# Performance work log

Measured on AMD Instinct MI355X. Metric: run time of the kernel, lower is better.

The kernel has to match this reference:

```python
import jax, jax.numpy as jnp
import numpy as np
from jax import lax

WIN = 9  # window size per spatial dim


def setup_inputs() -> dict:
    key = jax.random.key(0)
    k1, k2 = jax.random.split(key)
    shape = (2, 1, 160, 192, 160)  # [B, C=1, D, H, W]
    y_true = jax.random.uniform(k1, shape, dtype=jnp.float32)
    y_pred = jax.random.uniform(k2, shape, dtype=jnp.float32)
    return {"y_true": y_true, "y_pred": y_pred}


def reference(y_true, y_pred):
    Ii, Ji = y_true, y_pred
    ndims = Ii.ndim - 2  # 3 for volumes
    pad = WIN // 2
    # all five maps in the channel dim: [B, 5, D, H, W]
    all_five = jnp.concatenate([Ii, Ji, Ii * Ii, Ji * Ji, Ii * Ji], axis=1)
    # grouped box-filter conv: ones kernel [O=5, I/g=1, 9,9,9]
    kernel = jnp.ones((5, 1) + (WIN,) * ndims, dtype=Ii.dtype)
    conv = lax.conv_general_dilated(
        all_five, kernel,
        window_strides=(1,) * ndims,
        padding=[(pad, pad)] * ndims,
        feature_group_count=5,
        dimension_numbers=("NCDHW", "OIDHW", "NCDHW"),
    )
    I_sum, J_sum, I2_sum, J2_sum, IJ_sum = jnp.split(conv, 5, axis=1)
    win_size = jnp.asarray(float(WIN), dtype=Ii.dtype)
    cross = IJ_sum - J_sum / win_size * I_sum
    I_var = I2_sum - I_sum / win_size * I_sum
    J_var = J2_sum - J_sum / win_size * J_sum
    cc = cross * cross / (I_var * J_var + 1e-5)
    return -jnp.mean(cc)
```

## Files before the change

### kernel.cpp

```cpp
#include <hip/hip_runtime.h>

#define B_ 2
#define D_ 160
#define H_ 192
#define W_ 160
#define W4_ (W_ / 4)
#define HW_ (H_ * W_)
#define DHW_ (D_ * HW_)
#define NV_ ((long long)B_ * D_ * H_ * W_)

#define XT 32
#define NXT (W_ / XT)
#define YCH1 6
#define NYC1 (H_ / YCH1)
#define SPAD 4

#define ROWS2 8
#define ZCH2 10
#define NZC2 (D_ / ZCH2)
#define PAD 4
#define LROW (W_ + 2 * PAD)

#define A_YSTRIDE ((size_t)5 * W_)
#define A_ZSTRIDE ((size_t)5 * HW_)

typedef _Float16 half4 __attribute__((ext_vector_type(4)));

__global__ void k_zero(double* acc) { *acc = 0.0; }

__device__ __forceinline__ void add4h(float4& d, const half4 v) {
    d.x += (float)v.x; d.y += (float)v.y; d.z += (float)v.z; d.w += (float)v.w;
}
__device__ __forceinline__ void sub4h(float4& d, const half4 v) {
    d.x -= (float)v.x; d.y -= (float)v.y; d.z -= (float)v.z; d.w -= (float)v.w;
}

template<int SGN>
__device__ __forceinline__ void acc_lds(float4 s[5], const half4 ha, const half4 hb) {
    const float4 a = make_float4((float)ha.x, (float)ha.y, (float)ha.z, (float)ha.w);
    const float4 b = make_float4((float)hb.x, (float)hb.y, (float)hb.z, (float)hb.w);
    if (SGN > 0) {
        s[0].x += a.x;     s[0].y += a.y;     s[0].z += a.z;     s[0].w += a.w;
        s[1].x += b.x;     s[1].y += b.y;     s[1].z += b.z;     s[1].w += b.w;
        s[2].x += a.x*a.x; s[2].y += a.y*a.y; s[2].z += a.z*a.z; s[2].w += a.w*a.w;
        s[3].x += b.x*b.x; s[3].y += b.y*b.y; s[3].z += b.z*b.z; s[3].w += b.w*b.w;
        s[4].x += a.x*b.x; s[4].y += a.y*b.y; s[4].z += a.z*b.z; s[4].w += a.w*b.w;
    } else {
        s[0].x -= a.x;     s[0].y -= a.y;     s[0].z -= a.z;     s[0].w -= a.w;
        s[1].x -= b.x;     s[1].y -= b.y;     s[1].z -= b.z;     s[1].w -= b.w;
        s[2].x -= a.x*a.x; s[2].y -= a.y*a.y; s[2].z -= a.z*a.z; s[2].w -= a.w*a.w;
        s[3].x -= b.x*b.x; s[3].y -= b.y*b.y; s[3].z -= b.z*b.z; s[3].w -= b.w*b.w;
        s[4].x -= a.x*b.x; s[4].y -= a.y*b.y; s[4].z -= a.z*b.z; s[4].w -= a.w*b.w;
    }
}

__global__ __launch_bounds__(256) void k1_ysum(const float* __restrict__ I,
                                               const float* __restrict__ J,
                                               _Float16* __restrict__ A) {
    __shared__ _Float16 sI[H_][XT + SPAD];
    __shared__ _Float16 sJ[H_][XT + SPAD];
    const int tid = threadIdx.x;
    const int xt  = blockIdx.x % NXT;
    const int bz  = blockIdx.x / NXT;
    const int x0  = xt * XT;

    const float* Ibase = I + (size_t)bz * HW_ + x0;
    const float* Jbase = J + (size_t)bz * HW_ + x0;

#pragma unroll
    for (int i = 0; i < 6; ++i) {
        const int idx = i * 256 + tid;
        const int row = idx >> 3;
        const int g   = idx & 7;
        const float4 vi = *(const float4*)(Ibase + (size_t)row * W_ + g * 4);
        const float4 vj = *(const float4*)(Jbase + (size_t)row * W_ + g * 4);
        half4 hi, hj;
        hi.x = (_Float16)vi.x; hi.y = (_Float16)vi.y; hi.z = (_Float16)vi.z; hi.w = (_Float16)vi.w;
        hj.x = (_Float16)vj.x; hj.y = (_Float16)vj.y; hj.z = (_Float16)vj.z; hj.w = (_Float16)vj.w;
        *(half4*)&sI[row][g * 4] = hi;
        *(half4*)&sJ[row][g * 4] = hj;
    }
    __syncthreads();

    const int xg = tid & 7;
    const int yc = tid >> 3;
    const int y0 = yc * YCH1;
    const int x4 = xg * 4;

    _Float16* Ap = A + (size_t)bz * A_ZSTRIDE + x0 + x4;

    float4 s[5];
#pragma unroll
    for (int c = 0; c < 5; ++c) s[c] = make_float4(0, 0, 0, 0);

#pragma unroll
    for (int j = 0; j < 8; ++j) {
        const int yin = y0 - 4 + j;
        if (yin >= 0)
            acc_lds<+1>(s, *(const half4*)&sI[yin][x4], *(const half4*)&sJ[yin][x4]);
    }
#pragma unroll
    for (int k = 0; k < YCH1; ++k) {
        const int yi = y0 + k + 4;
        if (yi < H_)
            acc_lds<+1>(s, *(const half4*)&sI[yi][x4], *(const half4*)&sJ[yi][x4]);
        const int yo = y0 + k - 5;
        if (yo >= 0)
            acc_lds<-1>(s, *(const half4*)&sI[yo][x4], *(const half4*)&sJ[yo][x4]);

        _Float16* Ay = Ap + (size_t)(y0 + k) * A_YSTRIDE;
#pragma unroll
        for (int c = 0; c < 5; ++c) {
            half4 h;
            h.x = (_Float16)s[c].x; h.y = (_Float16)s[c].y;
            h.z = (_Float16)s[c].z; h.w = (_Float16)s[c].w;
            *(half4*)(Ay + c * W_) = h;
        }
    }
}

__global__ void k2_zxcc(const _Float16* __restrict__ A, double* __restrict__ acc) {
    __shared__ float sbuf[ROWS2][5][LROW];
    __shared__ float red[512];
    const int tid = threadIdx.x;
    const int r   = tid / W4_;
    const int l   = tid - r * W4_;
    const int x4  = l * 4;
    const int blk = blockIdx.x;
    const int zc  = blk % NZC2;
    const int rp  = blk / NZC2;
    const int gy  = rp * ROWS2 + r;
    const int b   = gy / H_;
    const int yy  = gy - b * H_;
    const int z0  = zc * ZCH2;

    {
        float* p = &sbuf[0][0][0];
        for (int i = tid; i < ROWS2 * 5 * LROW; i += ROWS2 * W4_) p[i] = 0.f;
    }

    const _Float16* Abase = A + (size_t)b * D_ * A_ZSTRIDE + (size_t)yy * A_YSTRIDE + x4;

    float4 s[5];
#pragma unroll
    for (int c = 0; c < 5; ++c) s[c] = make_float4(0, 0, 0, 0);
#pragma unroll
    for (int j = 0; j < 8; ++j) {
        const int zi = z0 - 4 + j;
        if (zi >= 0) {
            const _Float16* Az = Abase + (size_t)zi * A_ZSTRIDE;
#pragma unroll
            for (int c = 0; c < 5; ++c)
                add4h(s[c], *(const half4*)(Az + c * W_));
        }
    }
    __syncthreads();

    float local = 0.f;
    for (int k = 0; k < ZCH2; ++k) {
        const int zi = z0 + k + 4;
        if (zi < D_) {
            const _Float16* Az = Abase + (size_t)zi * A_ZSTRIDE;
#pragma unroll
            for (int c = 0; c < 5; ++c)
                add4h(s[c], *(const half4*)(Az + c * W_));
        }
        const int zo = z0 + k - 5;
        if (zo >= 0) {
            const _Float16* Az = Abase + (size_t)zo * A_ZSTRIDE;
#pragma unroll
            for (int c = 0; c < 5; ++c)
                sub4h(s[c], *(const half4*)(Az + c * W_));
        }
#pragma unroll
        for (int c = 0; c < 5; ++c)
            *(float4*)&sbuf[r][c][PAD + x4] = s[c];
        __syncthreads();

        float4 S5[5];
#pragma unroll
        for (int c = 0; c < 5; ++c) {
            const float4 a0 = *(const float4*)&sbuf[r][c][x4];
            const float4 a1 = *(const float4*)&sbuf[r][c][x4 + 4];
            const float4 a2 = *(const float4*)&sbuf[r][c][x4 + 8];
            const float o0 = a0.x + a0.y + a0.z + a0.w + a1.x + a1.y + a1.z + a1.w + a2.x;
            const float o1 = o0 - a0.x + a2.y;
            const float o2 = o1 - a0.y + a2.z;
            const float o3 = o2 - a0.z + a2.w;
            S5[c] = make_float4(o0, o1, o2, o3);
        }
        const float inv9 = 1.0f / 9.0f;
        {
            const float cr = S5[4].x - S5[1].x * S5[0].x * inv9;
            const float iv = S5[2].x - S5[0].x * S5[0].x * inv9;
            const float jv = S5[3].x - S5[1].x * S5[1].x * inv9;
            local += cr * cr / (iv * jv + 1e-5f);
        }
        {
            const float cr = S5[4].y - S5[1].y * S5[0].y * inv9;
            const float iv = S5[2].y - S5[0].y * S5[0].y * inv9;
            const float jv = S5[3].y - S5[1].y * S5[1].y * inv9;
            local += cr * cr / (iv * jv + 1e-5f);
        }
        {
            const float cr = S5[4].z - S5[1].z * S5[0].z * inv9;
            const float iv = S5[2].z - S5[0].z * S5[0].z * inv9;
            const float jv = S5[3].z - S5[1].z * S5[1].z * inv9;
            local += cr * cr / (iv * jv + 1e-5f);
        }
        {
            const float cr = S5[4].w - S5[1].w * S5[0].w * inv9;
            const float iv = S5[2].w - S5[0].w * S5[0].w * inv9;
            const float jv = S5[3].w - S5[1].w * S5[1].w * inv9;
            local += cr * cr / (iv * jv + 1e-5f);
        }
        __syncthreads();
    }

    red[tid] = local;
    if (tid < 192) red[320 + tid] = 0.f;
    __syncthreads();
    for (int off = 256; off > 0; off >>= 1) {
        if (tid < off) red[tid] += red[tid + off];
        __syncthreads();
    }
    if (tid == 0) atomicAdd(acc, (double)red[0]);
}

__global__ void p_direct(const float* __restrict__ I, const float* __restrict__ J,
                         double* __restrict__ acc) {
    const long long idx = (long long)blockIdx.x * blockDim.x + threadIdx.x;
    float local = 0.f;
    if (idx < NV_) {
        const int x = (int)(idx % W_);
        long long t = idx / W_;
        const int y = (int)(t % H_);
        t /= H_;
        const int z = (int)(t % D_);
        const int b = (int)(t / D_);
        const int z0 = max(z - 4, 0), z1 = min(z + 4, D_ - 1);
        const int y0 = max(y - 4, 0), y1 = min(y + 4, H_ - 1);
        const int x0 = max(x - 4, 0), x1 = min(x + 4, W_ - 1);
        float sI = 0.f, sJ = 0.f, sI2 = 0.f, sJ2 = 0.f, sIJ = 0.f;
        for (int zz = z0; zz <= z1; ++zz)
            for (int yy = y0; yy <= y1; ++yy) {
                const size_t row = ((size_t)(b * D_ + zz) * H_ + yy) * W_;
                for (int xx = x0; xx <= x1; ++xx) {
                    const float a = I[row + xx];
                    const float bb = J[row + xx];
                    sI += a; sJ += bb; sI2 += a * a; sJ2 += bb * bb; sIJ += a * bb;
                }
            }
        const float inv9 = 1.0f / 9.0f;
        const float cross = sIJ - sJ * sI * inv9;
        const float iv    = sI2 - sI * sI * inv9;
        const float jv    = sJ2 - sJ * sJ * inv9;
        local = cross * cross / (iv * jv + 1e-5f);
    }
    __shared__ float red[256];
    red[threadIdx.x] = local;
    __syncthreads();
    for (int off = 128; off > 0; off >>= 1) {
        if (threadIdx.x < off) red[threadIdx.x] += red[threadIdx.x + off];
        __syncthreads();
    }
    if (threadIdx.x == 0) atomicAdd(acc, (double)red[0]);
}

__global__ void k_final(const double* __restrict__ acc, float* __restrict__ out) {
    out[0] = (float)(-(*acc) / (double)NV_);
}

extern "C" void kernel_launch(void* const* d_in, const int* in_sizes, int n_in,
                              void* d_out, int out_size, void* d_ws, size_t ws_size,
                              hipStream_t stream) {
    const float* I = (const float*)d_in[0];
    const float* J = (const float*)d_in[1];
    float* out = (float*)d_out;

    const size_t needA = (size_t)5 * B_ * DHW_ * sizeof(_Float16);
    if (ws_size >= 1024 + needA) {
        double* acc = (double*)d_ws;
        _Float16* A = (_Float16*)((char*)d_ws + 1024);
        k_zero<<<1, 1, 0, stream>>>(acc);
        k1_ysum<<<B_ * D_ * NXT, 256, 0, stream>>>(I, J, A);
        k2_zxcc<<<NZC2 * (B_ * H_ / ROWS2), ROWS2 * W4_, 0, stream>>>(A, acc);
        k_final<<<1, 1, 0, stream>>>(acc, out);
    } else if (ws_size >= sizeof(double)) {
        double* acc = (double*)d_ws;
        k_zero<<<1, 1, 0, stream>>>(acc);
        p_direct<<<(int)((NV_ + 255) / 256), 256, 0, stream>>>(I, J, acc);
        k_final<<<1, 1, 0, stream>>>(acc, out);
    }
}
```

Before: 81.79 us.

## Retile y-sum kernel to full-width rows with half-height tiles and halo

The first-pass y-direction box-sum kernel now loads full 160-wide rows for half the H extent (96 rows plus an 8-row halo, zero-padded) instead of narrow 32-column strips over full H. Each of 320 threads sums a 12-row chunk without boundary branches. The aim is wider coalesced global loads, fewer blocks and less branching, at the cost of re-reading the halo rows and using more LDS per block. The z-prologue in the second kernel is also adjusted to start one plane earlier, which looks like a correctness fix to the window bookkeeping.

```diff
diff --git a/kernel.cpp b/kernel.cpp
--- a/kernel.cpp
+++ b/kernel.cpp
@@ -9,11 +9,11 @@
 #define DHW_ (D_ * HW_)
 #define NV_ ((long long)B_ * D_ * H_ * W_)
 
-#define XT 32
-#define NXT (W_ / XT)
-#define YCH1 6
-#define NYC1 (H_ / YCH1)
-#define SPAD 4
+#define YH1 96
+#define NYH (H_ / YH1)
+#define SROWS (YH1 + 8)
+#define SP 4
+#define YCH1 12
 
 #define ROWS2 8
 #define ZCH2 10
@@ -54,60 +54,63 @@
     }
 }
 
-__global__ __launch_bounds__(256) void k1_ysum(const float* __restrict__ I,
+__global__ __launch_bounds__(320) void k1_ysum(const float* __restrict__ I,
                                                const float* __restrict__ J,
                                                _Float16* __restrict__ A) {
-    __shared__ _Float16 sI[H_][XT + SPAD];
-    __shared__ _Float16 sJ[H_][XT + SPAD];
+    __shared__ _Float16 sI[SROWS][W_ + SP];
+    __shared__ _Float16 sJ[SROWS][W_ + SP];
     const int tid = threadIdx.x;
-    const int xt  = blockIdx.x % NXT;
-    const int bz  = blockIdx.x / NXT;
-    const int x0  = xt * XT;
-
-    const float* Ibase = I + (size_t)bz * HW_ + x0;
-    const float* Jbase = J + (size_t)bz * HW_ + x0;
-
-#pragma unroll
-    for (int i = 0; i < 6; ++i) {
-        const int idx = i * 256 + tid;
-        const int row = idx >> 3;
-        const int g   = idx & 7;
-        const float4 vi = *(const float4*)(Ibase + (size_t)row * W_ + g * 4);
-        const float4 vj = *(const float4*)(Jbase + (size_t)row * W_ + g * 4);
+    const int yh  = blockIdx.x % NYH;
+    const int bz  = blockIdx.x / NYH;
+    const int ylo = yh * YH1 - 4;
+
+    const float* Ib = I + (size_t)bz * HW_;
+    const float* Jb = J + (size_t)bz * HW_;
+
+#pragma unroll
+    for (int i = 0; i < 13; ++i) {
+        const int idx = i * 320 + tid;
+        const int lr  = idx / 40;
+        const int g   = idx - lr * 40;
+        const int gy  = ylo + lr;
         half4 hi, hj;
-        hi.x = (_Float16)vi.x; hi.y = (_Float16)vi.y; hi.z = (_Float16)vi.z; hi.w = (_Float16)vi.w;
-        hj.x = (_Float16)vj.x; hj.y = (_Float16)vj.y; hj.z = (_Float16)vj.z; hj.w = (_Float16)vj.w;
-        *(half4*)&sI[row][g * 4] = hi;
-        *(half4*)&sJ[row][g * 4] = hj;
-    }
-    __syncthreads();
-
-    const int xg = tid & 7;
-    const int yc = tid >> 3;
-    const int y0 = yc * YCH1;
+        hi.x = hi.y = hi.z = hi.w = (_Float16)0.f;
+        hj.x = hj.y = hj.z = hj.w = (_Float16)0.f;
+        if (gy >= 0 && gy < H_) {
+            const float4 vi = *(const float4*)(Ib + (size_t)gy * W_ + g * 4);
+            const float4 vj = *(const float4*)(Jb + (size_t)gy * W_ + g * 4);
+            hi.x = (_Float16)vi.x; hi.y = (_Float16)vi.y; hi.z = (_Float16)vi.z; hi.w = (_Float16)vi.w;
+            hj.x = (_Float16)vj.x; hj.y = (_Float16)vj.y; hj.z = (_Float16)vj.z; hj.w = (_Float16)vj.w;
+        }
+        *(half4*)&sI[lr][g * 4] = hi;
+        *(half4*)&sJ[lr][g * 4] = hj;
+    }
+    __syncthreads();
+
+    const int xg = tid % 40;
+    const int yc = tid / 40;
     const int x4 = xg * 4;
-
-    _Float16* Ap = A + (size_t)bz * A_ZSTRIDE + x0 + x4;
+    const int y0 = yh * YH1 + yc * YCH1;
+    const int l0 = y0 - ylo;
+
+    _Float16* Ap = A + (size_t)bz * A_ZSTRIDE + x4;
 
     float4 s[5];
 #pragma unroll
     for (int c = 0; c < 5; ++c) s[c] = make_float4(0, 0, 0, 0);
 
 #pragma unroll
-    for (int j = 0; j < 8; ++j) {
-        const int yin = y0 - 4 + j;
-        if (yin >= 0)
-            acc_lds<+1>(s, *(const half4*)&sI[yin][x4], *(const half4*)&sJ[yin][x4]);
-    }
+    for (int j = 0; j < 8; ++j)
+        acc_lds<+1>(s, *(const half4*)&sI[l0 - 4 + j][x4], *(const half4*)&sJ[l0 - 4 + j][x4]);
+
 #pragma unroll
     for (int k = 0; k < YCH1; ++k) {
-        const int yi = y0 + k + 4;
-        if (yi < H_)
-            acc_lds<+1>(s, *(const half4*)&sI[yi][x4], *(const half4*)&sJ[yi][x4]);
-        const int yo = y0 + k - 5;
-        if (yo >= 0)
-            acc_lds<-1>(s, *(const half4*)&sI[yo][x4], *(const half4*)&sJ[yo][x4]);
-
+        const int ll = l0 + k + 4;
+        acc_lds<+1>(s, *(const half4*)&sI[ll][x4], *(const half4*)&sJ[ll][x4]);
+        if (k >= 1) {
+            const int lt = l0 + k - 5;
+            acc_lds<-1>(s, *(const half4*)&sI[lt][x4], *(const half4*)&sJ[lt][x4]);
+        }
         _Float16* Ay = Ap + (size_t)(y0 + k) * A_YSTRIDE;
 #pragma unroll
         for (int c = 0; c < 5; ++c) {
@@ -145,8 +148,8 @@
 #pragma unroll
     for (int c = 0; c < 5; ++c) s[c] = make_float4(0, 0, 0, 0);
 #pragma unroll
-    for (int j = 0; j < 8; ++j) {
-        const int zi = z0 - 4 + j;
+    for (int j = 0; j < 9; ++j) {
+        const int zi = z0 - 5 + j;
         if (zi >= 0) {
             const _Float16* Az = Abase + (size_t)zi * A_ZSTRIDE;
 #pragma unroll
@@ -283,7 +286,7 @@
         double* acc = (double*)d_ws;
         _Float16* A = (_Float16*)((char*)d_ws + 1024);
         k_zero<<<1, 1, 0, stream>>>(acc);
-        k1_ysum<<<B_ * D_ * NXT, 256, 0, stream>>>(I, J, A);
+        k1_ysum<<<B_ * D_ * NYH, 320, 0, stream>>>(I, J, A);
         k2_zxcc<<<NZC2 * (B_ * H_ / ROWS2), ROWS2 * W4_, 0, stream>>>(A, acc);
         k_final<<<1, 1, 0, stream>>>(acc, out);
     } else if (ws_size >= sizeof(double)) {
```

After: 89.36 us. 1.09x slower.
